# Kernel optimization log

Measured on AMD Instinct MI355X. Metric: run time of the kernel, lower is better.

## Reference

```python
import jax, jax.numpy as jnp
import numpy as np

N = 100000          # number of road-network nodes
E = 640000          # number of directed edges (sparse adjacency nnz)
HID = 128           # hidden_dims = lane(16)+type(32)+length(16)+node(64)
N_LAYERS = 3        # hparams.baseline_gat_layer


def setup_inputs() -> dict:
    key = jax.random.key(0)
    ks = jax.random.split(key, 12)
    inp = {
        'node_feature': jax.random.randint(ks[0], (N,), 0, 100000),
        'type_feature': jax.random.randint(ks[1], (N,), 0, 20),
        'length_feature': jax.random.randint(ks[2], (N,), 0, 100),
        'lane_feature': jax.random.randint(ks[3], (N,), 0, 10),
        'adj_src': jax.random.randint(ks[4], (E,), 0, N),
        'adj_dst': jax.random.randint(ks[5], (E,), 0, N),
        'adj_val': jax.random.uniform(ks[6], (E,), dtype=jnp.float32),
        # learned parameters
        'node_emb': jax.random.normal(ks[7], (100000, 64), dtype=jnp.float32) * 0.02,
        'type_emb': jax.random.normal(ks[8], (20, 32), dtype=jnp.float32) * 0.02,
        'length_emb': jax.random.normal(ks[9], (100, 16), dtype=jnp.float32) * 0.02,
        'lane_emb': jax.random.normal(ks[10], (10, 16), dtype=jnp.float32) * 0.02,
        'W': jax.random.normal(ks[11], (HID, HID), dtype=jnp.float32) / np.sqrt(HID),
        'b': jnp.zeros((HID,), dtype=jnp.float32),
    }
    return inp


def spgcn_layer(x, W, b, adj_src, adj_dst, adj_val):
    # GCN layer: out = spmm(adj, x @ W) + b, adj given as COO edge list
    support = x @ W                                # [N, HID]
    msg = support[adj_src] * adj_val[:, None]      # gather + scale, [E, HID]
    agg = jax.ops.segment_sum(msg, adj_dst, num_segments=N)  # scatter-add
    return agg + b


def reference(node_feature, type_feature, length_feature, lane_feature,
              adj_src, adj_dst, adj_val,
              node_emb, type_emb, length_emb, lane_emb, W, b):
    # embedding lookups + concat: [lane, type, length, node] -> [N, HID]
    raw_feat = jnp.concatenate([
        lane_emb[lane_feature],
        type_emb[type_feature],
        length_emb[length_feature],
        node_emb[node_feature],
    ], axis=1)
    # repeated propagation with the SAME shared SPGCN layer weights
    for _ in range(N_LAYERS):
        raw_feat = spgcn_layer(raw_feat, W, b, adj_src, adj_dst, adj_val)
    return raw_feat
```

## Files before the change

kernel.cpp:

```cpp
#include <hip/hip_runtime.h>
#include <hip/hip_bf16.h>

typedef __hip_bfloat16 bf16;
typedef unsigned short ushort_t;
typedef __attribute__((ext_vector_type(8))) short short8;
typedef __attribute__((ext_vector_type(4))) float f32x4;

#define NN 100000
#define NE 640000
#define HD 128
#define NB 391
#define EMB_U 6250
#define HIST_U 2500
#define GEMM_U 782
#define AGG_U 6250
#define D_U 391
#define LDA 136


__device__ __forceinline__ float bf2f(ushort_t u) {
    unsigned v = (unsigned)u << 16;
    return __builtin_bit_cast(float, v);
}
__device__ __forceinline__ ushort_t f2bf(float f) {
    bf16 h = __float2bfloat16(f);
    return *(ushort_t*)&h;
}

struct P {
    const int *nodef, *typef, *lenf, *lanef, *adj_src, *adj_dst;
    const float *adj_val, *node_emb, *type_emb, *len_emb, *lane_emb, *W, *bias;
    ushort_t *Xa, *Xb, *w2t, *w3t;
    float *bw, *bw2, *d, *d2;
    int *cnt, *gtot, *offs, *slots;
    int2 *epack;
    float *outf;
};

__global__ __launch_bounds__(256) void ehist_k(P p) {
    __shared__ ushort_t WtL[HD * HD];
    __shared__ float bwS[HD];
    const int tid = threadIdx.x;
    if (blockIdx.x >= 1 + HIST_U) {
        const int idx = (blockIdx.x - 1 - HIST_U) * 256 + tid;
        const int i = idx >> 4;
        const int c = (idx & 15) * 8;
        const float* tbl; size_t base;
        if (c < 16)      { tbl = p.lane_emb; base = (size_t)p.lanef[i] * 16 + c; }
        else if (c < 48) { tbl = p.type_emb; base = (size_t)p.typef[i] * 32 + (c - 16); }
        else if (c < 64) { tbl = p.len_emb;  base = (size_t)p.lenf[i]  * 16 + (c - 48); }
        else             { tbl = p.node_emb; base = (size_t)p.nodef[i] * 64 + (c - 64); }
        const float4 f0 = *(const float4*)(tbl + base);
        const float4 f1 = *(const float4*)(tbl + base + 4);
        ushort_t u8[8] = { f2bf(f0.x), f2bf(f0.y), f2bf(f0.z), f2bf(f0.w),
                           f2bf(f1.x), f2bf(f1.y), f2bf(f1.z), f2bf(f1.w) };
        *(uint4*)(p.Xa + (size_t)i * HD + c) = *(uint4*)u8;
        return;
    }
    if (blockIdx.x >= 1) {
        const int e = (blockIdx.x - 1) * 256 + tid;
        p.slots[e] = atomicAdd(&p.cnt[p.adj_dst[e]], 1);
        return;
    }
    for (int i = tid; i < HD * HD / 4; i += 256) {
        const int k  = (i * 4) >> 7;
        const int n0 = (i * 4) & 127;
        const float4 f = *(const float4*)&p.W[(size_t)k * HD + n0];
        WtL[(n0 + 0) * HD + k] = f2bf(f.x);
        WtL[(n0 + 1) * HD + k] = f2bf(f.y);
        WtL[(n0 + 2) * HD + k] = f2bf(f.z);
        WtL[(n0 + 3) * HD + k] = f2bf(f.w);
    }
    __syncthreads();

    const int w = tid >> 6;
    const int ln = tid & 15;
    const int quad = (tid >> 4) & 3;
    const int koff = quad * 8;
    const f32x4 zero = {0.f, 0.f, 0.f, 0.f};

    short8 bfrg[2][4];
#pragma unroll
    for (int nt = 0; nt < 2; ++nt)
#pragma unroll
        for (int kc = 0; kc < 4; ++kc)
            bfrg[nt][kc] = *(const short8*)&WtL[(w * 32 + nt * 16 + ln) * HD + kc * 32 + koff];

#pragma unroll
    for (int mt = 0; mt < 8; ++mt) {
        const int m = mt * 16 + ln;
        short8 afrg[4];
#pragma unroll
        for (int kc = 0; kc < 4; ++kc) {
            ushort_t a[8];
#pragma unroll
            for (int j = 0; j < 8; ++j)
                a[j] = WtL[(kc * 32 + koff + j) * HD + m];
            afrg[kc] = *(short8*)a;
        }
        f32x4 acc[2] = {zero, zero};
#pragma unroll
        for (int nt = 0; nt < 2; ++nt)
#pragma unroll
            for (int kc = 0; kc < 4; ++kc)
                acc[nt] = __builtin_amdgcn_mfma_f32_16x16x32_bf16(
                        afrg[kc], bfrg[nt][kc], acc[nt], 0, 0, 0);
#pragma unroll
        for (int nt = 0; nt < 2; ++nt)
#pragma unroll
            for (int reg = 0; reg < 4; ++reg) {
                const int col = w * 32 + nt * 16 + ln;
                const int row = mt * 16 + quad * 4 + reg;
                p.w2t[col * HD + row] = f2bf(acc[nt][reg]);
            }
    }
    __syncthreads();

#pragma unroll
    for (int mt = 0; mt < 8; ++mt) {
        const int m = mt * 16 + ln;
        short8 afrg[4];
#pragma unroll
        for (int kc = 0; kc < 4; ++kc) {
            ushort_t a[8];
#pragma unroll
            for (int j = 0; j < 8; ++j)
                a[j] = p.w2t[(kc * 32 + koff + j) * HD + m];
            afrg[kc] = *(short8*)a;
        }
        f32x4 acc[2] = {zero, zero};
#pragma unroll
        for (int nt = 0; nt < 2; ++nt)
#pragma unroll
            for (int kc = 0; kc < 4; ++kc)
                acc[nt] = __builtin_amdgcn_mfma_f32_16x16x32_bf16(
                        afrg[kc], bfrg[nt][kc], acc[nt], 0, 0, 0);
#pragma unroll
        for (int nt = 0; nt < 2; ++nt)
#pragma unroll
            for (int reg = 0; reg < 4; ++reg) {
                const int col = w * 32 + nt * 16 + ln;
                const int row = mt * 16 + quad * 4 + reg;
                p.w3t[col * HD + row] = f2bf(acc[nt][reg]);
            }
    }
    __syncthreads();

    if (tid < HD) {
        float s = 0.f;
        for (int k = 0; k < HD; ++k) s += p.bias[k] * bf2f(WtL[tid * HD + k]);
        bwS[tid] = s;
        p.bw[tid] = s;
    }
    __syncthreads();
    if (tid < HD) {
        float s = 0.f;
        for (int k = 0; k < HD; ++k) s += bwS[k] * bf2f(WtL[tid * HD + k]);
        p.bw2[tid] = s;
    }
}

__global__ __launch_bounds__(256) void offs_k(P p) {
    const int idx = blockIdx.x * 256 + threadIdx.x;
    const int lane = threadIdx.x & 63;
    const int c = (idx < NN) ? p.cnt[idx] : 0;
    int pf = c;
#pragma unroll
    for (int o = 1; o < 64; o <<= 1) {
        const int x = __shfl_up(pf, o);
        if (lane >= o) pf += x;
    }
    int base = 0;
    if (lane == 63) base = atomicAdd(p.gtot, pf);
    base = __shfl(base, 63);
    if (idx < NN) p.offs[idx] = base + pf - c;
}

__global__ __launch_bounds__(256) void pos_k(P p) {
    const int e = blockIdx.x * 256 + threadIdx.x;
    const int dst = p.adj_dst[e];
    int2 pk;
    pk.x = p.adj_src[e];
    pk.y = __float_as_int(p.adj_val[e]);
    p.epack[p.offs[dst] + p.slots[e]] = pk;
}

__global__ __launch_bounds__(256) void agg_k(P p, const ushort_t* __restrict__ Xin,
                                             ushort_t* __restrict__ Xout, int aux) {
    if (blockIdx.x >= AGG_U) {
        const int node = (blockIdx.x - AGG_U) * 256 + threadIdx.x;
        if (node < NN) {
            const int lo = p.offs[node], hi = lo + p.cnt[node];
            float s = 0.f;
            if (aux == 1) {
                for (int j = lo; j < hi; ++j) s += __int_as_float(p.epack[j].y);
                p.d[node] = s;
            } else {
                for (int j = lo; j < hi; ++j) {
                    const int2 e = p.epack[j];
                    s += __int_as_float(e.y) * p.d[e.x];
                }
                p.d2[node] = s;
            }
        }
        return;
    }
    const int node = blockIdx.x * 16 + (threadIdx.x >> 4);
    const int lane = threadIdx.x & 15;
    const int c = lane * 8;
    const int lo = p.offs[node];
    const int hi = lo + p.cnt[node];
    float a0[8], a1[8], a2[8], a3[8];
#pragma unroll
    for (int k = 0; k < 8; ++k) { a0[k] = a1[k] = a2[k] = a3[k] = 0.f; }
    int j = lo;
    for (; j + 3 < hi; j += 4) {
        const int2 e0 = p.epack[j], e1 = p.epack[j + 1];
        const int2 e2 = p.epack[j + 2], e3 = p.epack[j + 3];
        const short8 u0 = *(const short8*)(Xin + (size_t)e0.x * HD + c);
        const short8 u1 = *(const short8*)(Xin + (size_t)e1.x * HD + c);
        const short8 u2 = *(const short8*)(Xin + (size_t)e2.x * HD + c);
        const short8 u3 = *(const short8*)(Xin + (size_t)e3.x * HD + c);
        const float v0 = __int_as_float(e0.y), v1 = __int_as_float(e1.y);
        const float v2 = __int_as_float(e2.y), v3 = __int_as_float(e3.y);
#pragma unroll
        for (int k = 0; k < 8; ++k) {
            a0[k] += bf2f((ushort_t)u0[k]) * v0;
            a1[k] += bf2f((ushort_t)u1[k]) * v1;
            a2[k] += bf2f((ushort_t)u2[k]) * v2;
            a3[k] += bf2f((ushort_t)u3[k]) * v3;
        }
    }
    for (; j < hi; ++j) {
        const int2 e0 = p.epack[j];
        const float v0 = __int_as_float(e0.y);
        const short8 u0 = *(const short8*)(Xin + (size_t)e0.x * HD + c);
#pragma unroll
        for (int k = 0; k < 8; ++k) a0[k] += bf2f((ushort_t)u0[k]) * v0;
    }
    ushort_t u8[8];
#pragma unroll
    for (int k = 0; k < 8; ++k) u8[k] = f2bf((a0[k] + a1[k]) + (a2[k] + a3[k]));
    *(uint4*)(Xout + (size_t)node * HD + c) = *(uint4*)u8;
}

__global__ __launch_bounds__(256) void gemmf_k(P p, const ushort_t* __restrict__ X2) {
    __shared__ ushort_t Xs[128 * LDA];
    const int tid = threadIdx.x;
    const int row0 = blockIdx.x * 128;

    {
        const int g = tid >> 4;
        const int lane = tid & 15;
        const int c = lane * 8;
        for (int mi = 0; mi < 8; ++mi) {
            const int m = g * 8 + mi;
            const int gm = row0 + m;
            float a0[8], a1[8], a2[8], a3[8];
#pragma unroll
            for (int k = 0; k < 8; ++k) { a0[k] = a1[k] = a2[k] = a3[k] = 0.f; }
            if (gm < NN) {
                const int lo = p.offs[gm];
                const int hi = lo + p.cnt[gm];
                int j = lo;
                for (; j + 3 < hi; j += 4) {
                    const int2 e0 = p.epack[j], e1 = p.epack[j + 1];
                    const int2 e2 = p.epack[j + 2], e3 = p.epack[j + 3];
                    const short8 u0 = *(const short8*)(X2 + (size_t)e0.x * HD + c);
                    const short8 u1 = *(const short8*)(X2 + (size_t)e1.x * HD + c);
                    const short8 u2 = *(const short8*)(X2 + (size_t)e2.x * HD + c);
                    const short8 u3 = *(const short8*)(X2 + (size_t)e3.x * HD + c);
                    const float v0 = __int_as_float(e0.y), v1 = __int_as_float(e1.y);
                    const float v2 = __int_as_float(e2.y), v3 = __int_as_float(e3.y);
#pragma unroll
                    for (int k = 0; k < 8; ++k) {
                        a0[k] += bf2f((ushort_t)u0[k]) * v0;
                        a1[k] += bf2f((ushort_t)u1[k]) * v1;
                        a2[k] += bf2f((ushort_t)u2[k]) * v2;
                        a3[k] += bf2f((ushort_t)u3[k]) * v3;
                    }
                }
                for (; j < hi; ++j) {
                    const int2 e0 = p.epack[j];
                    const float v0 = __int_as_float(e0.y);
                    const short8 u0 = *(const short8*)(X2 + (size_t)e0.x * HD + c);
#pragma unroll
                    for (int k = 0; k < 8; ++k) a0[k] += bf2f((ushort_t)u0[k]) * v0;
                }
            }
            ushort_t u8[8];
#pragma unroll
            for (int k = 0; k < 8; ++k) u8[k] = f2bf((a0[k] + a1[k]) + (a2[k] + a3[k]));
            *(uint4*)&Xs[m * LDA + c] = *(uint4*)u8;
        }
    }

    const int w = tid >> 6;
    const int ln = tid & 15;
    const int quad = (tid >> 4) & 3;
    const int koff = quad * 8;
    const int col0 = w * 32 + ln;
    const int col1 = col0 + 16;

    short8 bfrg[2][4];
#pragma unroll
    for (int nt = 0; nt < 2; ++nt)
#pragma unroll
        for (int kc = 0; kc < 4; ++kc)
            bfrg[nt][kc] = *(const short8*)&p.w3t[(size_t)(w * 32 + nt * 16 + ln) * HD + kc * 32 + koff];

    const float bwc0 = p.bw[col0],  bwc1 = p.bw[col1];
    const float bw2c0 = p.bw2[col0], bw2c1 = p.bw2[col1];
    const float bc0 = p.bias[col0], bc1 = p.bias[col1];

    __syncthreads();

    const f32x4 zero = {0.f, 0.f, 0.f, 0.f};
#pragma unroll
    for (int mt = 0; mt < 8; ++mt) {
        short8 afrg[4];
#pragma unroll
        for (int kc = 0; kc < 4; ++kc)
            afrg[kc] = *(const short8*)&Xs[(mt * 16 + ln) * LDA + kc * 32 + koff];
        f32x4 acc[2] = {zero, zero};
#pragma unroll
        for (int nt = 0; nt < 2; ++nt)
#pragma unroll
            for (int kc = 0; kc < 4; ++kc)
                acc[nt] = __builtin_amdgcn_mfma_f32_16x16x32_bf16(
                        afrg[kc], bfrg[nt][kc], acc[nt], 0, 0, 0);
#pragma unroll
        for (int reg = 0; reg < 4; ++reg) {
            const int gm = row0 + mt * 16 + quad * 4 + reg;
            if (gm < NN) {
                const float dg = p.d[gm], d2g = p.d2[gm];
                p.outf[(size_t)gm * HD + col0] = acc[0][reg] + d2g * bw2c0 + dg * bwc0 + bc0;
                p.outf[(size_t)gm * HD + col1] = acc[1][reg] + d2g * bw2c1 + dg * bwc1 + bc1;
            }
        }
    }
}

extern "C" void kernel_launch(void* const* d_in, const int* in_sizes, int n_in,
                              void* d_out, int out_size, void* d_ws, size_t ws_size,
                              hipStream_t stream) {
    P p;
    p.nodef    = (const int*)d_in[0];
    p.typef    = (const int*)d_in[1];
    p.lenf     = (const int*)d_in[2];
    p.lanef    = (const int*)d_in[3];
    p.adj_src  = (const int*)d_in[4];
    p.adj_dst  = (const int*)d_in[5];
    p.adj_val  = (const float*)d_in[6];
    p.node_emb = (const float*)d_in[7];
    p.type_emb = (const float*)d_in[8];
    p.len_emb  = (const float*)d_in[9];
    p.lane_emb = (const float*)d_in[10];
    p.W        = (const float*)d_in[11];
    p.bias     = (const float*)d_in[12];
    p.outf     = (float*)d_out;

    const size_t xbytes = (size_t)NN * HD * 2;
    char* wp = (char*)d_ws;
    p.Xa    = (ushort_t*)wp; wp += xbytes;
    p.Xb    = (ushort_t*)wp; wp += xbytes;
    p.cnt   = (int*)wp;      wp += (size_t)NN * 4;
    p.gtot  = (int*)wp;      wp += 16;
    p.offs  = (int*)wp;      wp += 400016;
    p.slots = (int*)wp;      wp += (size_t)NE * 4;
    p.epack = (int2*)wp;     wp += (size_t)NE * 8;
    p.w2t   = (ushort_t*)wp; wp += 32768;
    p.w3t   = (ushort_t*)wp; wp += 32768;
    p.bw    = (float*)wp;    wp += 512;
    p.bw2   = (float*)wp;    wp += 512;
    p.d     = (float*)wp;    wp += (size_t)NN * 4;
    p.d2    = (float*)wp;    wp += (size_t)NN * 4;

    hipMemsetAsync(p.cnt, 0, (size_t)NN * 4 + 16, stream);
    ehist_k<<<1 + HIST_U + EMB_U, 256, 0, stream>>>(p);
    offs_k<<<NB, 256, 0, stream>>>(p);
    pos_k<<<HIST_U, 256, 0, stream>>>(p);
    agg_k<<<AGG_U + D_U, 256, 0, stream>>>(p, p.Xa, p.Xb, 1);
    agg_k<<<AGG_U + D_U, 256, 0, stream>>>(p, p.Xb, p.Xa, 2);
    gemmf_k<<<GEMM_U, 256, 0, stream>>>(p, p.Xa);
}
```

Baseline: 304.4 us.

## Fuse offset scan and edge placement into one decoupled-lookback kernel

Replaces the separate offset-scan and edge-position kernels with a single kernel. Blocks take dynamic IDs from a counter; the first NB blocks run a block-wide exclusive scan with decoupled lookback flags to compute CSR offsets, then publish a per-block done flag. Every block then scatters its edges, spinning until the offset block its destination node belongs to is done. This removes one kernel launch and its boundary, and writes offs[NN] so consumers read hi from offs[node+1] instead of cnt. The cost is spin-waiting and forward-progress reliance on dynamic block ordering.

```diff
diff --git a/kernel.cpp b/kernel.cpp
--- a/kernel.cpp
+++ b/kernel.cpp
@@ -32,7 +32,8 @@
     const float *adj_val, *node_emb, *type_emb, *len_emb, *lane_emb, *W, *bias;
     ushort_t *Xa, *Xb, *w2t, *w3t;
     float *bw, *bw2, *d, *d2;
-    int *cnt, *gtot, *offs, *slots;
+    int *cnt, *ctr, *done, *offs, *slots;
+    unsigned *flagA;
     int2 *epack;
     float *outf;
 };
@@ -160,25 +161,76 @@
     }
 }
 
-__global__ __launch_bounds__(256) void offs_k(P p) {
-    const int idx = blockIdx.x * 256 + threadIdx.x;
-    const int lane = threadIdx.x & 63;
-    const int c = (idx < NN) ? p.cnt[idx] : 0;
-    int pf = c;
-#pragma unroll
-    for (int o = 1; o < 64; o <<= 1) {
-        const int x = __shfl_up(pf, o);
-        if (lane >= o) pf += x;
-    }
-    int base = 0;
-    if (lane == 63) base = atomicAdd(p.gtot, pf);
-    base = __shfl(base, 63);
-    if (idx < NN) p.offs[idx] = base + pf - c;
-}
-
-__global__ __launch_bounds__(256) void pos_k(P p) {
-    const int e = blockIdx.x * 256 + threadIdx.x;
+__global__ __launch_bounds__(256) void scanpos_k(P p) {
+    __shared__ int s[256];
+    __shared__ int sb_sh, run_sh;
+    const int tid = threadIdx.x;
+    if (tid == 0) sb_sh = atomicAdd(p.ctr, 1);
+    __syncthreads();
+    const int b = sb_sh;
+
+    if (b < NB) {
+        const int idx = b * 256 + tid;
+        const int v = (idx < NN) ? p.cnt[idx] : 0;
+        s[tid] = v;
+        __syncthreads();
+        for (int o = 1; o < 256; o <<= 1) {
+            const int x = (tid >= o) ? s[tid - o] : 0;
+            __syncthreads();
+            s[tid] += x;
+            __syncthreads();
+        }
+        const int total = s[255];
+        if (tid == 0)
+            __atomic_store_n(&p.flagA[b], (1u << 30) | (unsigned)total, __ATOMIC_RELEASE);
+        if (tid < 64) {
+            int run = 0;
+            if (b > 0) {
+                int j = b - 1;
+                for (;;) {
+                    const int m = j - tid;
+                    unsigned f = 0;
+                    if (m >= 0) {
+                        do {
+                            f = __atomic_load_n(&p.flagA[m], __ATOMIC_ACQUIRE);
+                        } while ((f >> 30) == 0u);
+                    }
+                    const bool hasP = (m >= 0) && ((f >> 30) == 2u);
+                    const unsigned long long pmask = __ballot(hasP);
+                    int contrib;
+                    if (pmask) {
+                        const int plane = __ffsll(pmask) - 1;
+                        contrib = (m >= 0 && tid <= plane) ? (int)(f & 0x3FFFFFFFu) : 0;
+                    } else {
+                        contrib = (m >= 0) ? (int)(f & 0x3FFFFFFFu) : 0;
+                    }
+                    for (int o = 32; o; o >>= 1) contrib += __shfl_down(contrib, o);
+                    contrib = __shfl(contrib, 0);
+                    run += contrib;
+                    if (pmask) break;
+                    j -= 64;
+                    if (j < 0) break;
+                }
+            }
+            if (tid == 0) {
+                __atomic_store_n(&p.flagA[b], (2u << 30) | (unsigned)(run + total), __ATOMIC_RELEASE);
+                run_sh = run;
+            }
+        }
+        __syncthreads();
+        const int run = run_sh;
+        if (idx <= NN) p.offs[idx] = run + s[tid] - v;
+        __syncthreads();
+        __threadfence();
+        if (tid == 0) __atomic_store_n(&p.done[b], 1, __ATOMIC_RELEASE);
+    }
+
+    const int e = b * 256 + tid;
     const int dst = p.adj_dst[e];
+    const int r = dst >> 8;
+    while (__atomic_load_n(&p.done[r], __ATOMIC_ACQUIRE) == 0)
+        __builtin_amdgcn_s_sleep(2);
+    __threadfence();
     int2 pk;
     pk.x = p.adj_src[e];
     pk.y = __float_as_int(p.adj_val[e]);
@@ -190,7 +242,7 @@
     if (blockIdx.x >= AGG_U) {
         const int node = (blockIdx.x - AGG_U) * 256 + threadIdx.x;
         if (node < NN) {
-            const int lo = p.offs[node], hi = lo + p.cnt[node];
+            const int lo = p.offs[node], hi = p.offs[node + 1];
             float s = 0.f;
             if (aux == 1) {
                 for (int j = lo; j < hi; ++j) s += __int_as_float(p.epack[j].y);
@@ -209,7 +261,7 @@
     const int lane = threadIdx.x & 15;
     const int c = lane * 8;
     const int lo = p.offs[node];
-    const int hi = lo + p.cnt[node];
+    const int hi = p.offs[node + 1];
     float a0[8], a1[8], a2[8], a3[8];
 #pragma unroll
     for (int k = 0; k < 8; ++k) { a0[k] = a1[k] = a2[k] = a3[k] = 0.f; }
@@ -261,7 +313,7 @@
             for (int k = 0; k < 8; ++k) { a0[k] = a1[k] = a2[k] = a3[k] = 0.f; }
             if (gm < NN) {
                 const int lo = p.offs[gm];
-                const int hi = lo + p.cnt[gm];
+                const int hi = p.offs[gm + 1];
                 int j = lo;
                 for (; j + 3 < hi; j += 4) {
                     const int2 e0 = p.epack[j], e1 = p.epack[j + 1];
@@ -365,7 +417,9 @@
     p.Xa    = (ushort_t*)wp; wp += xbytes;
     p.Xb    = (ushort_t*)wp; wp += xbytes;
     p.cnt   = (int*)wp;      wp += (size_t)NN * 4;
-    p.gtot  = (int*)wp;      wp += 16;
+    p.ctr   = (int*)wp;      wp += 16;
+    p.flagA = (unsigned*)wp; wp += 1600;
+    p.done  = (int*)wp;      wp += 1600;
     p.offs  = (int*)wp;      wp += 400016;
     p.slots = (int*)wp;      wp += (size_t)NE * 4;
     p.epack = (int2*)wp;     wp += (size_t)NE * 8;
@@ -376,10 +430,9 @@
     p.d     = (float*)wp;    wp += (size_t)NN * 4;
     p.d2    = (float*)wp;    wp += (size_t)NN * 4;
 
-    hipMemsetAsync(p.cnt, 0, (size_t)NN * 4 + 16, stream);
+    hipMemsetAsync(p.cnt, 0, (size_t)NN * 4 + 16 + 1600 + 1600, stream);
     ehist_k<<<1 + HIST_U + EMB_U, 256, 0, stream>>>(p);
-    offs_k<<<NB, 256, 0, stream>>>(p);
-    pos_k<<<HIST_U, 256, 0, stream>>>(p);
+    scanpos_k<<<HIST_U, 256, 0, stream>>>(p);
     agg_k<<<AGG_U + D_U, 256, 0, stream>>>(p, p.Xa, p.Xb, 1);
     agg_k<<<AGG_U + D_U, 256, 0, stream>>>(p, p.Xb, p.Xa, 2);
     gemmf_k<<<GEMM_U, 256, 0, stream>>>(p, p.Xa);
```

Measured after the change: 1.089 ms. +257.7%, slower.
